# Optimization experiments

Measured on AMD Instinct MI355X. Metric: run time of the kernel, lower is better.

Reference implementation:

```python
import jax, jax.numpy as jnp
import numpy as np

B, N, D, H = 4, 2048, 256, 8
d = D // H          # 32 per-head dim
EPS = 1e-5
SCALE = 1.0 / float(np.sqrt(d))


def setup_inputs() -> dict:
    key = jax.random.key(0)
    ks = jax.random.split(key, 6)
    s = 0.02
    x = jax.random.normal(ks[0], (B, N, D), jnp.float32)
    # RoPE frequencies: theta_j = 10000^(-2j/d), angle = pos * theta
    inv_freq = 1.0 / (10000.0 ** (jnp.arange(0, d, 2, dtype=jnp.float32) / d))  # (d/2,)
    ang = jnp.arange(N, dtype=jnp.float32)[:, None] * inv_freq[None, :]          # (N, d/2)
    return {
        "x": x,
        "freqs_cos": jnp.cos(ang),
        "freqs_sin": jnp.sin(ang),
        "w_qkv": jax.random.normal(ks[1], (D, 3 * D), jnp.float32) * s,
        "b_qkv": jnp.zeros((3 * D,), jnp.float32),
        "w_proj": jax.random.normal(ks[2], (D, D), jnp.float32) * s,
        "b_proj": jnp.zeros((D,), jnp.float32),
        "ln1_g": jnp.ones((D,), jnp.float32),
        "ln1_b": jnp.zeros((D,), jnp.float32),
        "ln2_g": jnp.ones((D,), jnp.float32),
        "ln2_b": jnp.zeros((D,), jnp.float32),
        "w1": jax.random.normal(ks[3], (D, 2 * D), jnp.float32) * s,
        "b1": jnp.zeros((2 * D,), jnp.float32),
        "w2": jax.random.normal(ks[4], (2 * D, D), jnp.float32) * s,
        "b2": jnp.zeros((D,), jnp.float32),
    }


def _layer_norm(x, g, b):
    mu = jnp.mean(x, axis=-1, keepdims=True)
    var = jnp.mean(jnp.square(x - mu), axis=-1, keepdims=True)
    return (x - mu) * jax.lax.rsqrt(var + EPS) * g + b


def _rope(t, cos, sin):
    # t: (B,H,N,d); interleaved (even,odd) pairs viewed as complex, multiplied by e^{i*ang}
    tr = t.reshape(B, H, N, d // 2, 2)
    te, to = tr[..., 0], tr[..., 1]
    c = cos[None, None, :, :]
    s = sin[None, None, :, :]
    oe = te * c - to * s
    oo = te * s + to * c
    return jnp.stack([oe, oo], axis=-1).reshape(B, H, N, d)


def reference(x, freqs_cos, freqs_sin, w_qkv, b_qkv, w_proj, b_proj,
              ln1_g, ln1_b, ln2_g, ln2_b, w1, b1, w2, b2):
    # Pre-LN MHSA with RoPE (dropout = identity at eval)
    h = _layer_norm(x, ln1_g, ln1_b)
    qkv = (h @ w_qkv + b_qkv).reshape(B, N, 3, H, d).transpose(0, 2, 3, 1, 4)  # (B,3,H,N,d)
    q, k, v = qkv[:, 0], qkv[:, 1], qkv[:, 2]
    q = _rope(q, freqs_cos, freqs_sin)
    k = _rope(k, freqs_cos, freqs_sin)
    attn = jax.nn.softmax(jnp.einsum('bhnd,bhmd->bhnm', q, k) * SCALE, axis=-1)
    out = jnp.einsum('bhnm,bhmd->bhnd', attn, v).transpose(0, 2, 1, 3).reshape(B, N, D)
    x = x + (out @ w_proj + b_proj)
    h = _layer_norm(x, ln2_g, ln2_b)
    ffn = jax.nn.relu(h @ w1 + b1) @ w2 + b2
    return x + ffn
```

## Files before the change

kernel.cpp:

```cpp
#include <hip/hip_runtime.h>
#include <hip/hip_bf16.h>
#include <math.h>

#define Bsz 4
#define Nseq 2048
#define Dm 256
#define Hh 8
#define Hd 32
#define EPS_ 1e-5f
#define SCALE_ 0.17677669529663687f

typedef __attribute__((ext_vector_type(8))) short short8;
typedef __attribute__((ext_vector_type(4))) short short4v;
typedef __attribute__((ext_vector_type(4))) float f32x4;

__device__ __forceinline__ void gload16(const void* g, void* l) {
    __builtin_amdgcn_global_load_lds(
        (const __attribute__((address_space(1))) void*)g,
        (__attribute__((address_space(3))) void*)l, 16, 0, 0);
}

__device__ __forceinline__ short8 read8x2(const __hip_bfloat16* p) {
    short4v lo = *(const short4v*)p;
    short4v hi = *(const short4v*)(p + 4);
    return __builtin_shufflevector(lo, hi, 0, 1, 2, 3, 4, 5, 6, 7);
}

__global__ __launch_bounds__(256) void ln_kernel(const float* __restrict__ x,
                                                 const float* __restrict__ g,
                                                 const float* __restrict__ b,
                                                 __hip_bfloat16* __restrict__ out) {
    int row  = blockIdx.x * 4 + (threadIdx.x >> 6);
    int lane = threadIdx.x & 63;
    const float* xr = x + (size_t)row * Dm;
    float4 v = *(const float4*)(xr + lane * 4);
    float s  = v.x + v.y + v.z + v.w;
    float ss = v.x * v.x + v.y * v.y + v.z * v.z + v.w * v.w;
    #pragma unroll
    for (int off = 32; off; off >>= 1) {
        s  += __shfl_xor(s, off);
        ss += __shfl_xor(ss, off);
    }
    float mu  = s * (1.0f / Dm);
    float var = ss * (1.0f / Dm) - mu * mu;
    float rs  = rsqrtf(var + EPS_);
    float4 gv = *(const float4*)(g + lane * 4);
    float4 bv = *(const float4*)(b + lane * 4);
    float o0 = (v.x - mu) * rs * gv.x + bv.x;
    float o1 = (v.y - mu) * rs * gv.y + bv.y;
    float o2 = (v.z - mu) * rs * gv.z + bv.z;
    float o3 = (v.w - mu) * rs * gv.w + bv.w;
    __hip_bfloat16 h0 = __float2bfloat16(o0), h1 = __float2bfloat16(o1);
    __hip_bfloat16 h2 = __float2bfloat16(o2), h3 = __float2bfloat16(o3);
    short4v o4 = { *(short*)&h0, *(short*)&h1, *(short*)&h2, *(short*)&h3 };
    *(short4v*)(out + (size_t)row * Dm + lane * 4) = o4;
}

__global__ __launch_bounds__(256) void wconv_kernel(
    const float* __restrict__ s0, const float* __restrict__ s1,
    const float* __restrict__ s2, const float* __restrict__ s3,
    __hip_bfloat16* __restrict__ d0, __hip_bfloat16* __restrict__ d1,
    __hip_bfloat16* __restrict__ d2, __hip_bfloat16* __restrict__ d3) {
    __shared__ float t[32][33];
    int bid = blockIdx.x;
    const float* src; __hip_bfloat16* dst; int K, N, tb;
    if (bid < 192)      { src = s0; dst = d0; K = 256; N = 768; tb = bid; }
    else if (bid < 256) { src = s1; dst = d1; K = 256; N = 256; tb = bid - 192; }
    else if (bid < 384) { src = s2; dst = d2; K = 256; N = 512; tb = bid - 256; }
    else                { src = s3; dst = d3; K = 512; N = 256; tb = bid - 384; }
    int tn = N >> 5;
    int k0 = (tb / tn) * 32, n0 = (tb % tn) * 32;
    int c = threadIdx.x & 31, r0 = threadIdx.x >> 5;
    #pragma unroll
    for (int i = 0; i < 4; i++) {
        int r = r0 + i * 8;
        t[r][c] = src[(size_t)(k0 + r) * N + n0 + c];
    }
    __syncthreads();
    #pragma unroll
    for (int i = 0; i < 4; i++) {
        int n = r0 + i * 8;
        dst[(size_t)(n0 + n) * K + k0 + c] = __float2bfloat16(t[c][n]);
    }
}

template <int EPI>
__global__ __launch_bounds__(256) void mfma_gemm(const __hip_bfloat16* __restrict__ A,
                                                 const __hip_bfloat16* __restrict__ Wt,
                                                 const float* __restrict__ bias,
                                                 const float* __restrict__ res,
                                                 float* __restrict__ Cf,
                                                 __hip_bfloat16* __restrict__ Cb,
                                                 int M, int Nn, int K) {
    __shared__ __align__(16) __hip_bfloat16 As[128 * 32];
    __shared__ __align__(16) __hip_bfloat16 Bs[64 * 32];
    const int tid = threadIdx.x, w = tid >> 6, lane = tid & 63;
    const int lm = lane & 15, lq = lane >> 4;
    const int bm = blockIdx.y * 128, bn = blockIdx.x * 64;
    f32x4 acc[2][4];
    #pragma unroll
    for (int i = 0; i < 2; i++)
        #pragma unroll
        for (int j = 0; j < 4; j++) acc[i][j] = (f32x4){0.f, 0.f, 0.f, 0.f};

    const int sw = (lq ^ (lm & 3)) * 8;
    for (int k0 = 0; k0 < K; k0 += 32) {
        #pragma unroll
        for (int p = 0; p < 2; p++) {
            int c = p * 256 + w * 64 + lane;
            int r = c >> 2, gk = ((c & 3) ^ (r & 3)) * 8;
            gload16(A + (size_t)(bm + r) * K + k0 + gk, As + (p * 256 + w * 64) * 8);
        }
        {
            int c = w * 64 + lane;
            int r = c >> 2, gk = ((c & 3) ^ (r & 3)) * 8;
            gload16(Wt + (size_t)(bn + r) * K + k0 + gk, Bs + (w * 64) * 8);
        }
        __syncthreads();
        short8 a0 = *(const short8*)&As[(w * 32 + lm) * 32 + sw];
        short8 a1 = *(const short8*)&As[(w * 32 + 16 + lm) * 32 + sw];
        #pragma unroll
        for (int nf = 0; nf < 4; nf++) {
            short8 bfr = *(const short8*)&Bs[(nf * 16 + lm) * 32 + sw];
            acc[0][nf] = __builtin_amdgcn_mfma_f32_16x16x32_bf16(a0, bfr, acc[0][nf], 0, 0, 0);
            acc[1][nf] = __builtin_amdgcn_mfma_f32_16x16x32_bf16(a1, bfr, acc[1][nf], 0, 0, 0);
        }
        __syncthreads();
    }
    #pragma unroll
    for (int nf = 0; nf < 4; nf++) {
        int cg = bn + nf * 16 + lm;
        float bi = bias[cg];
        #pragma unroll
        for (int mf = 0; mf < 2; mf++) {
            #pragma unroll
            for (int r = 0; r < 4; r++) {
                int rg = bm + w * 32 + mf * 16 + lq * 4 + r;
                float v = acc[mf][nf][r] + bi;
                if (EPI == 1) {
                    v = fmaxf(v, 0.f);
                    Cb[(size_t)rg * Nn + cg] = __float2bfloat16(v);
                } else {
                    v += res[(size_t)rg * Nn + cg];
                    Cf[(size_t)rg * Nn + cg] = v;
                }
            }
        }
    }
}

__global__ __launch_bounds__(256) void qkv_mfma(const __hip_bfloat16* __restrict__ A,
                                                const __hip_bfloat16* __restrict__ Wt,
                                                const float* __restrict__ bias,
                                                const float* __restrict__ fcos,
                                                const float* __restrict__ fsin,
                                                __hip_bfloat16* __restrict__ qout,
                                                __hip_bfloat16* __restrict__ kout,
                                                __hip_bfloat16* __restrict__ vout) {
    const int K = 256, Nn = 768;
    __shared__ __align__(16) __hip_bfloat16 As[128 * 32];
    __shared__ __align__(16) __hip_bfloat16 Bs[64 * 32];
    __shared__ __align__(16) float cosS[2048];
    __shared__ __align__(16) float sinS[2048];
    const int tid = threadIdx.x, w = tid >> 6, lane = tid & 63;
    const int lm = lane & 15, lq = lane >> 4;
    const int bm = blockIdx.y * 128, bn = blockIdx.x * 64;
    f32x4 acc[2][4];
    #pragma unroll
    for (int i = 0; i < 2; i++)
        #pragma unroll
        for (int j = 0; j < 4; j++) acc[i][j] = (f32x4){0.f, 0.f, 0.f, 0.f};

    const int sw = (lq ^ (lm & 3)) * 8;
    for (int k0 = 0; k0 < K; k0 += 32) {
        #pragma unroll
        for (int p = 0; p < 2; p++) {
            int c = p * 256 + w * 64 + lane;
            int r = c >> 2, gk = ((c & 3) ^ (r & 3)) * 8;
            gload16(A + (size_t)(bm + r) * K + k0 + gk, As + (p * 256 + w * 64) * 8);
        }
        {
            int c = w * 64 + lane;
            int r = c >> 2, gk = ((c & 3) ^ (r & 3)) * 8;
            gload16(Wt + (size_t)(bn + r) * K + k0 + gk, Bs + (w * 64) * 8);
        }
        __syncthreads();
        short8 a0 = *(const short8*)&As[(w * 32 + lm) * 32 + sw];
        short8 a1 = *(const short8*)&As[(w * 32 + 16 + lm) * 32 + sw];
        #pragma unroll
        for (int nf = 0; nf < 4; nf++) {
            short8 bfr = *(const short8*)&Bs[(nf * 16 + lm) * 32 + sw];
            acc[0][nf] = __builtin_amdgcn_mfma_f32_16x16x32_bf16(a0, bfr, acc[0][nf], 0, 0, 0);
            acc[1][nf] = __builtin_amdgcn_mfma_f32_16x16x32_bf16(a1, bfr, acc[1][nf], 0, 0, 0);
        }
        __syncthreads();
    }
    int n0 = bm & (Nseq - 1);
    *(float4*)&cosS[tid * 8]     = *(const float4*)&fcos[n0 * 16 + tid * 8];
    *(float4*)&cosS[tid * 8 + 4] = *(const float4*)&fcos[n0 * 16 + tid * 8 + 4];
    *(float4*)&sinS[tid * 8]     = *(const float4*)&fsin[n0 * 16 + tid * 8];
    *(float4*)&sinS[tid * 8 + 4] = *(const float4*)&fsin[n0 * 16 + tid * 8 + 4];
    __syncthreads();

    const int seg = bn >> 8;
    #pragma unroll
    for (int nf = 0; nf < 4; nf++) {
        int cg = bn + nf * 16 + lm;
        int hh = (cg & 255) >> 5;
        int dd = (nf & 1) * 16 + lm;
        int i0 = dd >> 1;
        float bi = bias[cg];
        #pragma unroll
        for (int mf = 0; mf < 2; mf++) {
            #pragma unroll
            for (int r = 0; r < 4; r++) {
                int rg = bm + w * 32 + mf * 16 + lq * 4 + r;
                int nl = rg - bm;
                float v = acc[mf][nf][r] + bi;
                float vp = __shfl_xor(v, 1);
                float outv;
                if (seg < 2) {
                    float cs = cosS[nl * 16 + i0], sn = sinS[nl * 16 + i0];
                    outv = (dd & 1) ? (vp * sn + v * cs) : (v * cs - vp * sn);
                    if (seg == 0) outv *= SCALE_;
                } else {
                    outv = v;
                }
                int bb = rg >> 11, n = rg & (Nseq - 1);
                __hip_bfloat16* dst = (seg == 0) ? qout : ((seg == 1) ? kout : vout);
                dst[(((size_t)(bb * Hh + hh)) * Nseq + n) * Hd + dd] = __float2bfloat16(outv);
            }
        }
    }
}

__global__ __launch_bounds__(256) void attn_mfma(const __hip_bfloat16* __restrict__ q,
                                                 const __hip_bfloat16* __restrict__ k,
                                                 const __hip_bfloat16* __restrict__ v,
                                                 __hip_bfloat16* __restrict__ att) {
    __shared__ __align__(16) __hip_bfloat16 Qs[64 * 32];
    __shared__ __align__(16) __hip_bfloat16 Ks[2][64 * 32];
    __shared__ __align__(16) __hip_bfloat16 Vt[2][32 * 68];
    __shared__ __align__(16) __hip_bfloat16 Ps[4][16 * 68];
    const int tid = threadIdx.x, w = tid >> 6, lane = tid & 63;
    const int lm = lane & 15, lq = lane >> 4;
    const int bh = blockIdx.y, qbase = blockIdx.x * 64;
    const __hip_bfloat16* qp = q + ((size_t)bh * Nseq + qbase) * Hd;
    const __hip_bfloat16* kp = k + (size_t)bh * Nseq * Hd;
    const __hip_bfloat16* vp = v + (size_t)bh * Nseq * Hd;
    const int srow = tid >> 2, sc = tid & 3;
    const int ssw = (sc ^ (srow & 3)) * 8;

    *(float4*)&Qs[srow * 32 + sc * 8] = *(const float4*)(qp + srow * 32 + ssw);
    {
        float4 k4 = *(const float4*)(kp + srow * 32 + ssw);
        float4 v4 = *(const float4*)(vp + (size_t)srow * Hd + sc * 8);
        *(float4*)&Ks[0][srow * 32 + sc * 8] = k4;
        const __hip_bfloat16* vv = (const __hip_bfloat16*)&v4;
        #pragma unroll
        for (int j = 0; j < 8; j++) Vt[0][(sc * 8 + j) * 68 + srow] = vv[j];
    }
    __syncthreads();

    const int sw = (lq ^ (lm & 3)) * 8;
    short8 qf = *(const short8*)&Qs[(w * 16 + lm) * 32 + sw];
    f32x4 O0 = {0.f, 0.f, 0.f, 0.f};
    f32x4 O1 = {0.f, 0.f, 0.f, 0.f};
    float sm[4] = {0.f, 0.f, 0.f, 0.f};

    for (int kt = 0; kt < Nseq / 64; kt++) {
        int cur = kt & 1;
        if (kt + 1 < Nseq / 64) {
            const __hip_bfloat16* kpn = kp + (size_t)(kt + 1) * 64 * Hd;
            float4 k4 = *(const float4*)(kpn + srow * 32 + ssw);
            float4 v4 = *(const float4*)(vp + (size_t)((kt + 1) * 64 + srow) * Hd + sc * 8);
            *(float4*)&Ks[cur ^ 1][srow * 32 + sc * 8] = k4;
            const __hip_bfloat16* vv = (const __hip_bfloat16*)&v4;
            #pragma unroll
            for (int j = 0; j < 8; j++) Vt[cur ^ 1][(sc * 8 + j) * 68 + srow] = vv[j];
        }
        f32x4 S[4];
        #pragma unroll
        for (int kb = 0; kb < 4; kb++) {
            short8 kf = *(const short8*)&Ks[cur][(kb * 16 + lm) * 32 + sw];
            f32x4 zz = {0.f, 0.f, 0.f, 0.f};
            S[kb] = __builtin_amdgcn_mfma_f32_16x16x32_bf16(qf, kf, zz, 0, 0, 0);
        }
        #pragma unroll
        for (int kb = 0; kb < 4; kb++) {
            #pragma unroll
            for (int r = 0; r < 4; r++) {
                float p = __expf(S[kb][r]);
                sm[r] += p;
                Ps[w][(lq * 4 + r) * 68 + kb * 16 + lm] = __float2bfloat16(p);
            }
        }
        #pragma unroll
        for (int sub = 0; sub < 2; sub++) {
            short8 pf  = read8x2(&Ps[w][lm * 68 + sub * 32 + lq * 8]);
            short8 vf0 = read8x2(&Vt[cur][lm * 68 + sub * 32 + lq * 8]);
            short8 vf1 = read8x2(&Vt[cur][(16 + lm) * 68 + sub * 32 + lq * 8]);
            O0 = __builtin_amdgcn_mfma_f32_16x16x32_bf16(pf, vf0, O0, 0, 0, 0);
            O1 = __builtin_amdgcn_mfma_f32_16x16x32_bf16(pf, vf1, O1, 0, 0, 0);
        }
        __syncthreads();
    }
    #pragma unroll
    for (int off = 1; off <= 8; off <<= 1) {
        #pragma unroll
        for (int r = 0; r < 4; r++) sm[r] += __shfl_xor(sm[r], off);
    }
    const int bb = bh >> 3, hh = bh & 7;
    #pragma unroll
    for (int r = 0; r < 4; r++) {
        float inv = 1.0f / sm[r];
        int n = qbase + w * 16 + lq * 4 + r;
        __hip_bfloat16* op = att + ((size_t)(bb * Nseq + n)) * Dm + hh * Hd;
        op[lm]      = __float2bfloat16(O0[r] * inv);
        op[16 + lm] = __float2bfloat16(O1[r] * inv);
    }
}

extern "C" void kernel_launch(void* const* d_in, const int* in_sizes, int n_in,
                              void* d_out, int out_size, void* d_ws, size_t ws_size,
                              hipStream_t stream) {
    const float* x      = (const float*)d_in[0];
    const float* fcos   = (const float*)d_in[1];
    const float* fsin   = (const float*)d_in[2];
    const float* w_qkv  = (const float*)d_in[3];
    const float* b_qkv  = (const float*)d_in[4];
    const float* w_proj = (const float*)d_in[5];
    const float* b_proj = (const float*)d_in[6];
    const float* ln1_g  = (const float*)d_in[7];
    const float* ln1_b  = (const float*)d_in[8];
    const float* ln2_g  = (const float*)d_in[9];
    const float* ln2_b  = (const float*)d_in[10];
    const float* w1     = (const float*)d_in[11];
    const float* b1     = (const float*)d_in[12];
    const float* w2     = (const float*)d_in[13];
    const float* b2     = (const float*)d_in[14];
    float* out = (float*)d_out;
    char* base = (char*)d_ws;
    const size_t MB = (size_t)1 << 20;

    __hip_bfloat16* h   = (__hip_bfloat16*)(base);
    float*          x2f = (float*)(base);
    __hip_bfloat16* qb  = (__hip_bfloat16*)(base + 8 * MB);
    __hip_bfloat16* kbf = (__hip_bfloat16*)(base + 12 * MB);
    __hip_bfloat16* vbf = (__hip_bfloat16*)(base + 16 * MB);
    __hip_bfloat16* att = (__hip_bfloat16*)(base + 20 * MB);
    __hip_bfloat16* h2  = (__hip_bfloat16*)(base + 8 * MB);
    __hip_bfloat16* ffn = (__hip_bfloat16*)(base + 24 * MB);
    __hip_bfloat16* wqT = (__hip_bfloat16*)(base + 32 * MB);
    __hip_bfloat16* wpT = (__hip_bfloat16*)(base + 32 * MB + 393216);
    __hip_bfloat16* w1T = (__hip_bfloat16*)(base + 32 * MB + 524288);
    __hip_bfloat16* w2T = (__hip_bfloat16*)(base + 32 * MB + 786432);

    const int rows = Bsz * Nseq;

    wconv_kernel<<<512, 256, 0, stream>>>(w_qkv, w_proj, w1, w2, wqT, wpT, w1T, w2T);
    ln_kernel<<<rows / 4, 256, 0, stream>>>(x, ln1_g, ln1_b, h);
    qkv_mfma<<<dim3(12, 64), 256, 0, stream>>>(h, wqT, b_qkv, fcos, fsin, qb, kbf, vbf);
    attn_mfma<<<dim3(Nseq / 64, Bsz * Hh), 256, 0, stream>>>(qb, kbf, vbf, att);
    mfma_gemm<2><<<dim3(4, 64), 256, 0, stream>>>(att, wpT, b_proj, x, x2f, nullptr,
                                                  rows, 256, 256);
    ln_kernel<<<rows / 4, 256, 0, stream>>>(x2f, ln2_g, ln2_b, h2);
    mfma_gemm<1><<<dim3(8, 64), 256, 0, stream>>>(h2, w1T, b1, nullptr, nullptr, ffn,
                                                  rows, 512, 256);
    mfma_gemm<2><<<dim3(4, 64), 256, 0, stream>>>(ffn, w2T, b2, x2f, out, nullptr,
                                                  rows, 256, 512);
}
```

Before: 192.6 us.

## Fuse LayerNorm into QKV/FFN1 GEMMs, pre-transpose V, shrink proj/FFN2 tiles

LayerNorm is folded into the QKV and FFN1 GEMM prologues: per-row statistics are computed into shared memory and the A tile is normalized and converted to bf16 on the fly, which removes two separate LN kernels and their bf16 intermediates. The QKV epilogue writes V already transposed, so attention can load V fragments straight into registers and load Q/K with async global-to-LDS copies instead of scattering into LDS. The proj and FFN2 GEMMs move to 64-row tiles to double the block count. In exchange each QKV/FFN1 block re-reads fp32 x from global memory for every output column tile, and the RoPE tables are now read from global memory instead of shared memory.

After: 230.3 us. 1.2x slower.

```diff
diff --git a/kernel.cpp b/kernel.cpp
--- a/kernel.cpp
+++ b/kernel.cpp
@@ -26,34 +26,9 @@
     return __builtin_shufflevector(lo, hi, 0, 1, 2, 3, 4, 5, 6, 7);
 }
 
-__global__ __launch_bounds__(256) void ln_kernel(const float* __restrict__ x,
-                                                 const float* __restrict__ g,
-                                                 const float* __restrict__ b,
-                                                 __hip_bfloat16* __restrict__ out) {
-    int row  = blockIdx.x * 4 + (threadIdx.x >> 6);
-    int lane = threadIdx.x & 63;
-    const float* xr = x + (size_t)row * Dm;
-    float4 v = *(const float4*)(xr + lane * 4);
-    float s  = v.x + v.y + v.z + v.w;
-    float ss = v.x * v.x + v.y * v.y + v.z * v.z + v.w * v.w;
-    #pragma unroll
-    for (int off = 32; off; off >>= 1) {
-        s  += __shfl_xor(s, off);
-        ss += __shfl_xor(ss, off);
-    }
-    float mu  = s * (1.0f / Dm);
-    float var = ss * (1.0f / Dm) - mu * mu;
-    float rs  = rsqrtf(var + EPS_);
-    float4 gv = *(const float4*)(g + lane * 4);
-    float4 bv = *(const float4*)(b + lane * 4);
-    float o0 = (v.x - mu) * rs * gv.x + bv.x;
-    float o1 = (v.y - mu) * rs * gv.y + bv.y;
-    float o2 = (v.z - mu) * rs * gv.z + bv.z;
-    float o3 = (v.w - mu) * rs * gv.w + bv.w;
-    __hip_bfloat16 h0 = __float2bfloat16(o0), h1 = __float2bfloat16(o1);
-    __hip_bfloat16 h2 = __float2bfloat16(o2), h3 = __float2bfloat16(o3);
-    short4v o4 = { *(short*)&h0, *(short*)&h1, *(short*)&h2, *(short*)&h3 };
-    *(short4v*)(out + (size_t)row * Dm + lane * 4) = o4;
+__device__ __forceinline__ short bf16s(float f) {
+    __hip_bfloat16 h = __float2bfloat16(f);
+    return *(short*)&h;
 }
 
 __global__ __launch_bounds__(256) void wconv_kernel(
@@ -84,7 +59,7 @@
     }
 }
 
-template <int EPI>
+template <int TM, int EPI>
 __global__ __launch_bounds__(256) void mfma_gemm(const __hip_bfloat16* __restrict__ A,
                                                  const __hip_bfloat16* __restrict__ Wt,
                                                  const float* __restrict__ bias,
@@ -92,38 +67,41 @@
                                                  float* __restrict__ Cf,
                                                  __hip_bfloat16* __restrict__ Cb,
                                                  int M, int Nn, int K) {
-    __shared__ __align__(16) __hip_bfloat16 As[128 * 32];
+    constexpr int MF = TM / 64;
+    __shared__ __align__(16) __hip_bfloat16 As[TM * 32];
     __shared__ __align__(16) __hip_bfloat16 Bs[64 * 32];
     const int tid = threadIdx.x, w = tid >> 6, lane = tid & 63;
     const int lm = lane & 15, lq = lane >> 4;
-    const int bm = blockIdx.y * 128, bn = blockIdx.x * 64;
-    f32x4 acc[2][4];
-    #pragma unroll
-    for (int i = 0; i < 2; i++)
+    const int bm = blockIdx.y * TM, bn = blockIdx.x * 64;
+    f32x4 acc[MF][4];
+    #pragma unroll
+    for (int i = 0; i < MF; i++)
         #pragma unroll
         for (int j = 0; j < 4; j++) acc[i][j] = (f32x4){0.f, 0.f, 0.f, 0.f};
 
     const int sw = (lq ^ (lm & 3)) * 8;
     for (int k0 = 0; k0 < K; k0 += 32) {
         #pragma unroll
-        for (int p = 0; p < 2; p++) {
-            int c = p * 256 + w * 64 + lane;
+        for (int p = 0; p < MF; p++) {
+            int c = p * 256 + tid;
             int r = c >> 2, gk = ((c & 3) ^ (r & 3)) * 8;
             gload16(A + (size_t)(bm + r) * K + k0 + gk, As + (p * 256 + w * 64) * 8);
         }
         {
-            int c = w * 64 + lane;
-            int r = c >> 2, gk = ((c & 3) ^ (r & 3)) * 8;
-            gload16(Wt + (size_t)(bn + r) * K + k0 + gk, Bs + (w * 64) * 8);
-        }
-        __syncthreads();
-        short8 a0 = *(const short8*)&As[(w * 32 + lm) * 32 + sw];
-        short8 a1 = *(const short8*)&As[(w * 32 + 16 + lm) * 32 + sw];
+            int r = tid >> 2, gk = ((tid & 3) ^ (r & 3)) * 8;
+            gload16(Wt + (size_t)(bn + r) * K + k0 + gk, Bs + w * 512);
+        }
+        __syncthreads();
+        short8 a[MF];
+        #pragma unroll
+        for (int mf = 0; mf < MF; mf++)
+            a[mf] = *(const short8*)&As[(w * (TM / 4) + mf * 16 + lm) * 32 + sw];
         #pragma unroll
         for (int nf = 0; nf < 4; nf++) {
             short8 bfr = *(const short8*)&Bs[(nf * 16 + lm) * 32 + sw];
-            acc[0][nf] = __builtin_amdgcn_mfma_f32_16x16x32_bf16(a0, bfr, acc[0][nf], 0, 0, 0);
-            acc[1][nf] = __builtin_amdgcn_mfma_f32_16x16x32_bf16(a1, bfr, acc[1][nf], 0, 0, 0);
+            #pragma unroll
+            for (int mf = 0; mf < MF; mf++)
+                acc[mf][nf] = __builtin_amdgcn_mfma_f32_16x16x32_bf16(a[mf], bfr, acc[mf][nf], 0, 0, 0);
         }
         __syncthreads();
     }
@@ -132,10 +110,10 @@
         int cg = bn + nf * 16 + lm;
         float bi = bias[cg];
         #pragma unroll
-        for (int mf = 0; mf < 2; mf++) {
+        for (int mf = 0; mf < MF; mf++) {
             #pragma unroll
             for (int r = 0; r < 4; r++) {
-                int rg = bm + w * 32 + mf * 16 + lq * 4 + r;
+                int rg = bm + w * (TM / 4) + mf * 16 + lq * 4 + r;
                 float v = acc[mf][nf][r] + bi;
                 if (EPI == 1) {
                     v = fmaxf(v, 0.f);
@@ -149,22 +127,48 @@
     }
 }
 
-__global__ __launch_bounds__(256) void qkv_mfma(const __hip_bfloat16* __restrict__ A,
-                                                const __hip_bfloat16* __restrict__ Wt,
-                                                const float* __restrict__ bias,
-                                                const float* __restrict__ fcos,
-                                                const float* __restrict__ fsin,
-                                                __hip_bfloat16* __restrict__ qout,
-                                                __hip_bfloat16* __restrict__ kout,
-                                                __hip_bfloat16* __restrict__ vout) {
-    const int K = 256, Nn = 768;
+__global__ __launch_bounds__(256) void qkv_fused(const float* __restrict__ x,
+                                                 const __hip_bfloat16* __restrict__ Wt,
+                                                 const float* __restrict__ bias,
+                                                 const float* __restrict__ g,
+                                                 const float* __restrict__ bvec,
+                                                 const float* __restrict__ fcos,
+                                                 const float* __restrict__ fsin,
+                                                 __hip_bfloat16* __restrict__ qout,
+                                                 __hip_bfloat16* __restrict__ kout,
+                                                 __hip_bfloat16* __restrict__ vt) {
+    const int K = 256;
     __shared__ __align__(16) __hip_bfloat16 As[128 * 32];
     __shared__ __align__(16) __hip_bfloat16 Bs[64 * 32];
-    __shared__ __align__(16) float cosS[2048];
-    __shared__ __align__(16) float sinS[2048];
+    __shared__ float muS[128], rsS[128];
     const int tid = threadIdx.x, w = tid >> 6, lane = tid & 63;
     const int lm = lane & 15, lq = lane >> 4;
     const int bm = blockIdx.y * 128, bn = blockIdx.x * 64;
+
+    #pragma unroll
+    for (int i = 0; i < 8; i++) {
+        int r = w * 32 + i * 4 + (lane >> 4);
+        const float* xr = x + (size_t)(bm + r) * 256 + (lane & 15) * 16;
+        float s = 0.f, ss = 0.f;
+        #pragma unroll
+        for (int j = 0; j < 4; j++) {
+            float4 v = *(const float4*)(xr + j * 4);
+            s  += v.x + v.y + v.z + v.w;
+            ss += v.x * v.x + v.y * v.y + v.z * v.z + v.w * v.w;
+        }
+        #pragma unroll
+        for (int off = 1; off <= 8; off <<= 1) {
+            s  += __shfl_xor(s, off);
+            ss += __shfl_xor(ss, off);
+        }
+        if ((lane & 15) == 0) {
+            float mu = s * (1.0f / 256.0f);
+            muS[r] = mu;
+            rsS[r] = rsqrtf(ss * (1.0f / 256.0f) - mu * mu + EPS_);
+        }
+    }
+    __syncthreads();
+
     f32x4 acc[2][4];
     #pragma unroll
     for (int i = 0; i < 2; i++)
@@ -173,16 +177,40 @@
 
     const int sw = (lq ^ (lm & 3)) * 8;
     for (int k0 = 0; k0 < K; k0 += 32) {
+        short8 hbuf[2];
+        int rr[2];
         #pragma unroll
         for (int p = 0; p < 2; p++) {
-            int c = p * 256 + w * 64 + lane;
+            int c = p * 256 + tid;
             int r = c >> 2, gk = ((c & 3) ^ (r & 3)) * 8;
-            gload16(A + (size_t)(bm + r) * K + k0 + gk, As + (p * 256 + w * 64) * 8);
+            rr[p] = r;
+            const float* src = x + (size_t)(bm + r) * 256 + k0 + gk;
+            float4 f0 = *(const float4*)src;
+            float4 f1 = *(const float4*)(src + 4);
+            float4 g0 = *(const float4*)(g + k0 + gk);
+            float4 g1 = *(const float4*)(g + k0 + gk + 4);
+            float4 b0 = *(const float4*)(bvec + k0 + gk);
+            float4 b1 = *(const float4*)(bvec + k0 + gk + 4);
+            float mu = muS[r], rs = rsS[r];
+            short8 h;
+            h[0] = bf16s((f0.x - mu) * rs * g0.x + b0.x);
+            h[1] = bf16s((f0.y - mu) * rs * g0.y + b0.y);
+            h[2] = bf16s((f0.z - mu) * rs * g0.z + b0.z);
+            h[3] = bf16s((f0.w - mu) * rs * g0.w + b0.w);
+            h[4] = bf16s((f1.x - mu) * rs * g1.x + b1.x);
+            h[5] = bf16s((f1.y - mu) * rs * g1.y + b1.y);
+            h[6] = bf16s((f1.z - mu) * rs * g1.z + b1.z);
+            h[7] = bf16s((f1.w - mu) * rs * g1.w + b1.w);
+            hbuf[p] = h;
         }
         {
-            int c = w * 64 + lane;
-            int r = c >> 2, gk = ((c & 3) ^ (r & 3)) * 8;
-            gload16(Wt + (size_t)(bn + r) * K + k0 + gk, Bs + (w * 64) * 8);
+            int r = tid >> 2, gk = ((tid & 3) ^ (r & 3)) * 8;
+            gload16(Wt + (size_t)(bn + r) * K + k0 + gk, Bs + w * 512);
+        }
+        #pragma unroll
+        for (int p = 0; p < 2; p++) {
+            int c = p * 256 + tid;
+            *(short8*)&As[(rr[p] * 4 + (c & 3)) * 8] = hbuf[p];
         }
         __syncthreads();
         short8 a0 = *(const short8*)&As[(w * 32 + lm) * 32 + sw];
@@ -195,13 +223,6 @@
         }
         __syncthreads();
     }
-    int n0 = bm & (Nseq - 1);
-    *(float4*)&cosS[tid * 8]     = *(const float4*)&fcos[n0 * 16 + tid * 8];
-    *(float4*)&cosS[tid * 8 + 4] = *(const float4*)&fcos[n0 * 16 + tid * 8 + 4];
-    *(float4*)&sinS[tid * 8]     = *(const float4*)&fsin[n0 * 16 + tid * 8];
-    *(float4*)&sinS[tid * 8 + 4] = *(const float4*)&fsin[n0 * 16 + tid * 8 + 4];
-    __syncthreads();
-
     const int seg = bn >> 8;
     #pragma unroll
     for (int nf = 0; nf < 4; nf++) {
@@ -215,20 +236,127 @@
             #pragma unroll
             for (int r = 0; r < 4; r++) {
                 int rg = bm + w * 32 + mf * 16 + lq * 4 + r;
-                int nl = rg - bm;
+                int bb = rg >> 11, n = rg & (Nseq - 1);
                 float v = acc[mf][nf][r] + bi;
-                float vp = __shfl_xor(v, 1);
-                float outv;
-                if (seg < 2) {
-                    float cs = cosS[nl * 16 + i0], sn = sinS[nl * 16 + i0];
-                    outv = (dd & 1) ? (vp * sn + v * cs) : (v * cs - vp * sn);
+                if (seg == 2) {
+                    vt[(((size_t)(bb * Hh + hh)) * Hd + dd) * Nseq + n] = __float2bfloat16(v);
+                } else {
+                    float vp = __shfl_xor(v, 1);
+                    float cs = fcos[n * 16 + i0], sn = fsin[n * 16 + i0];
+                    float outv = (dd & 1) ? (vp * sn + v * cs) : (v * cs - vp * sn);
                     if (seg == 0) outv *= SCALE_;
-                } else {
-                    outv = v;
+                    __hip_bfloat16* dst = (seg == 0) ? qout : kout;
+                    dst[(((size_t)(bb * Hh + hh)) * Nseq + n) * Hd + dd] = __float2bfloat16(outv);
                 }
-                int bb = rg >> 11, n = rg & (Nseq - 1);
-                __hip_bfloat16* dst = (seg == 0) ? qout : ((seg == 1) ? kout : vout);
-                dst[(((size_t)(bb * Hh + hh)) * Nseq + n) * Hd + dd] = __float2bfloat16(outv);
+            }
+        }
+    }
+}
+
+__global__ __launch_bounds__(256) void ffn1_fused(const float* __restrict__ x,
+                                                  const __hip_bfloat16* __restrict__ Wt,
+                                                  const float* __restrict__ bias,
+                                                  const float* __restrict__ g,
+                                                  const float* __restrict__ bvec,
+                                                  __hip_bfloat16* __restrict__ Cb,
+                                                  int Nn) {
+    const int K = 256;
+    __shared__ __align__(16) __hip_bfloat16 As[128 * 32];
+    __shared__ __align__(16) __hip_bfloat16 Bs[64 * 32];
+    __shared__ float muS[128], rsS[128];
+    const int tid = threadIdx.x, w = tid >> 6, lane = tid & 63;
+    const int lm = lane & 15, lq = lane >> 4;
+    const int bm = blockIdx.y * 128, bn = blockIdx.x * 64;
+
+    #pragma unroll
+    for (int i = 0; i < 8; i++) {
+        int r = w * 32 + i * 4 + (lane >> 4);
+        const float* xr = x + (size_t)(bm + r) * 256 + (lane & 15) * 16;
+        float s = 0.f, ss = 0.f;
+        #pragma unroll
+        for (int j = 0; j < 4; j++) {
+            float4 v = *(const float4*)(xr + j * 4);
+            s  += v.x + v.y + v.z + v.w;
+            ss += v.x * v.x + v.y * v.y + v.z * v.z + v.w * v.w;
+        }
+        #pragma unroll
+        for (int off = 1; off <= 8; off <<= 1) {
+            s  += __shfl_xor(s, off);
+            ss += __shfl_xor(ss, off);
+        }
+        if ((lane & 15) == 0) {
+            float mu = s * (1.0f / 256.0f);
+            muS[r] = mu;
+            rsS[r] = rsqrtf(ss * (1.0f / 256.0f) - mu * mu + EPS_);
+        }
+    }
+    __syncthreads();
+
+    f32x4 acc[2][4];
+    #pragma unroll
+    for (int i = 0; i < 2; i++)
+        #pragma unroll
+        for (int j = 0; j < 4; j++) acc[i][j] = (f32x4){0.f, 0.f, 0.f, 0.f};
+
+    const int sw = (lq ^ (lm & 3)) * 8;
+    for (int k0 = 0; k0 < K; k0 += 32) {
+        short8 hbuf[2];
+        int rr[2];
+        #pragma unroll
+        for (int p = 0; p < 2; p++) {
+            int c = p * 256 + tid;
+            int r = c >> 2, gk = ((c & 3) ^ (r & 3)) * 8;
+            rr[p] = r;
+            const float* src = x + (size_t)(bm + r) * 256 + k0 + gk;
+            float4 f0 = *(const float4*)src;
+            float4 f1 = *(const float4*)(src + 4);
+            float4 g0 = *(const float4*)(g + k0 + gk);
+            float4 g1 = *(const float4*)(g + k0 + gk + 4);
+            float4 b0 = *(const float4*)(bvec + k0 + gk);
+            float4 b1 = *(const float4*)(bvec + k0 + gk + 4);
+            float mu = muS[r], rs = rsS[r];
+            short8 h;
+            h[0] = bf16s((f0.x - mu) * rs * g0.x + b0.x);
+            h[1] = bf16s((f0.y - mu) * rs * g0.y + b0.y);
+            h[2] = bf16s((f0.z - mu) * rs * g0.z + b0.z);
+            h[3] = bf16s((f0.w - mu) * rs * g0.w + b0.w);
+            h[4] = bf16s((f1.x - mu) * rs * g1.x + b1.x);
+            h[5] = bf16s((f1.y - mu) * rs * g1.y + b1.y);
+            h[6] = bf16s((f1.z - mu) * rs * g1.z + b1.z);
+            h[7] = bf16s((f1.w - mu) * rs * g1.w + b1.w);
+            hbuf[p] = h;
+        }
+        {
+            int r = tid >> 2, gk = ((tid & 3) ^ (r & 3)) * 8;
+            gload16(Wt + (size_t)(bn + r) * K + k0 + gk, Bs + w * 512);
+        }
+        #pragma unroll
+        for (int p = 0; p < 2; p++) {
+            int c = p * 256 + tid;
+            *(short8*)&As[(rr[p] * 4 + (c & 3)) * 8] = hbuf[p];
+        }
+        __syncthreads();
+        short8 a0 = *(const short8*)&As[(w * 32 + lm) * 32 + sw];
+        short8 a1 = *(const short8*)&As[(w * 32 + 16 + lm) * 32 + sw];
+        #pragma unroll
+        for (int nf = 0; nf < 4; nf++) {
+            short8 bfr = *(const short8*)&Bs[(nf * 16 + lm) * 32 + sw];
+            acc[0][nf] = __builtin_amdgcn_mfma_f32_16x16x32_bf16(a0, bfr, acc[0][nf], 0, 0, 0);
+            acc[1][nf] = __builtin_amdgcn_mfma_f32_16x16x32_bf16(a1, bfr, acc[1][nf], 0, 0, 0);
+        }
+        __syncthreads();
+    }
+    #pragma unroll
+    for (int nf = 0; nf < 4; nf++) {
+        int cg = bn + nf * 16 + lm;
+        float bi = bias[cg];
+        #pragma unroll
+        for (int mf = 0; mf < 2; mf++) {
+            #pragma unroll
+            for (int r = 0; r < 4; r++) {
+                int rg = bm + w * 32 + mf * 16 + lq * 4 + r;
+                float v = fmaxf(acc[mf][nf][r] + bi, 0.f);
+                Cb[(size_t)rg * Nn + cg] = __float2bfloat16(v);
             }
         }
     }
@@ -236,30 +364,26 @@
 
 __global__ __launch_bounds__(256) void attn_mfma(const __hip_bfloat16* __restrict__ q,
                                                  const __hip_bfloat16* __restrict__ k,
-                                                 const __hip_bfloat16* __restrict__ v,
+                                                 const __hip_bfloat16* __restrict__ vt,
                                                  __hip_bfloat16* __restrict__ att) {
     __shared__ __align__(16) __hip_bfloat16 Qs[64 * 32];
     __shared__ __align__(16) __hip_bfloat16 Ks[2][64 * 32];
-    __shared__ __align__(16) __hip_bfloat16 Vt[2][32 * 68];
     __shared__ __align__(16) __hip_bfloat16 Ps[4][16 * 68];
     const int tid = threadIdx.x, w = tid >> 6, lane = tid & 63;
     const int lm = lane & 15, lq = lane >> 4;
     const int bh = blockIdx.y, qbase = blockIdx.x * 64;
-    const __hip_bfloat16* qp = q + ((size_t)bh * Nseq + qbase) * Hd;
-    const __hip_bfloat16* kp = k + (size_t)bh * Nseq * Hd;
-    const __hip_bfloat16* vp = v + (size_t)bh * Nseq * Hd;
-    const int srow = tid >> 2, sc = tid & 3;
-    const int ssw = (sc ^ (srow & 3)) * 8;
-
-    *(float4*)&Qs[srow * 32 + sc * 8] = *(const float4*)(qp + srow * 32 + ssw);
-    {
-        float4 k4 = *(const float4*)(kp + srow * 32 + ssw);
-        float4 v4 = *(const float4*)(vp + (size_t)srow * Hd + sc * 8);
-        *(float4*)&Ks[0][srow * 32 + sc * 8] = k4;
-        const __hip_bfloat16* vv = (const __hip_bfloat16*)&v4;
-        #pragma unroll
-        for (int j = 0; j < 8; j++) Vt[0][(sc * 8 + j) * 68 + srow] = vv[j];
-    }
+    const __hip_bfloat16* qp  = q + ((size_t)bh * Nseq + qbase) * Hd;
+    const __hip_bfloat16* kp  = k + (size_t)bh * Nseq * Hd;
+    const __hip_bfloat16* vr0 = vt + ((size_t)bh * Hd + lm) * Nseq + lq * 8;
+    const __hip_bfloat16* vr1 = vr0 + 16 * Nseq;
+
+    const int sr = tid >> 2, sgk = ((tid & 3) ^ (sr & 3)) * 8;
+    gload16(qp + sr * 32 + sgk, Qs + w * 512);
+    gload16(kp + sr * 32 + sgk, Ks[0] + w * 512);
+    short8 v00 = *(const short8*)(vr0);
+    short8 v01 = *(const short8*)(vr0 + 32);
+    short8 v10 = *(const short8*)(vr1);
+    short8 v11 = *(const short8*)(vr1 + 32);
     __syncthreads();
 
     const int sw = (lq ^ (lm & 3)) * 8;
@@ -270,14 +394,14 @@
 
     for (int kt = 0; kt < Nseq / 64; kt++) {
         int cur = kt & 1;
+        short8 n00, n01, n10, n11;
         if (kt + 1 < Nseq / 64) {
-            const __hip_bfloat16* kpn = kp + (size_t)(kt + 1) * 64 * Hd;
-            float4 k4 = *(const float4*)(kpn + srow * 32 + ssw);
-            float4 v4 = *(const float4*)(vp + (size_t)((kt + 1) * 64 + srow) * Hd + sc * 8);
-            *(float4*)&Ks[cur ^ 1][srow * 32 + sc * 8] = k4;
-            const __hip_bfloat16* vv = (const __hip_bfloat16*)&v4;
-            #pragma unroll
-            for (int j = 0; j < 8; j++) Vt[cur ^ 1][(sc * 8 + j) * 68 + srow] = vv[j];
+            gload16(kp + (size_t)(kt + 1) * 64 * 32 + sr * 32 + sgk, Ks[cur ^ 1] + w * 512);
+            int kb = (kt + 1) * 64;
+            n00 = *(const short8*)(vr0 + kb);
+            n01 = *(const short8*)(vr0 + kb + 32);
+            n10 = *(const short8*)(vr1 + kb);
+            n11 = *(const short8*)(vr1 + kb + 32);
         }
         f32x4 S[4];
         #pragma unroll
@@ -295,14 +419,13 @@
                 Ps[w][(lq * 4 + r) * 68 + kb * 16 + lm] = __float2bfloat16(p);
             }
         }
-        #pragma unroll
-        for (int sub = 0; sub < 2; sub++) {
-            short8 pf  = read8x2(&Ps[w][lm * 68 + sub * 32 + lq * 8]);
-            short8 vf0 = read8x2(&Vt[cur][lm * 68 + sub * 32 + lq * 8]);
-            short8 vf1 = read8x2(&Vt[cur][(16 + lm) * 68 + sub * 32 + lq * 8]);
-            O0 = __builtin_amdgcn_mfma_f32_16x16x32_bf16(pf, vf0, O0, 0, 0, 0);
-            O1 = __builtin_amdgcn_mfma_f32_16x16x32_bf16(pf, vf1, O1, 0, 0, 0);
-        }
+        short8 pf0 = read8x2(&Ps[w][lm * 68 + lq * 8]);
+        short8 pf1 = read8x2(&Ps[w][lm * 68 + 32 + lq * 8]);
+        O0 = __builtin_amdgcn_mfma_f32_16x16x32_bf16(pf0, v00, O0, 0, 0, 0);
+        O1 = __builtin_amdgcn_mfma_f32_16x16x32_bf16(pf0, v10, O1, 0, 0, 0);
+        O0 = __builtin_amdgcn_mfma_f32_16x16x32_bf16(pf1, v01, O0, 0, 0, 0);
+        O1 = __builtin_amdgcn_mfma_f32_16x16x32_bf16(pf1, v11, O1, 0, 0, 0);
+        v00 = n00; v01 = n01; v10 = n10; v11 = n11;
         __syncthreads();
     }
     #pragma unroll
@@ -343,13 +466,11 @@
     char* base = (char*)d_ws;
     const size_t MB = (size_t)1 << 20;
 
-    __hip_bfloat16* h   = (__hip_bfloat16*)(base);
-    float*          x2f = (float*)(base);
-    __hip_bfloat16* qb  = (__hip_bfloat16*)(base + 8 * MB);
-    __hip_bfloat16* kbf = (__hip_bfloat16*)(base + 12 * MB);
-    __hip_bfloat16* vbf = (__hip_bfloat16*)(base + 16 * MB);
-    __hip_bfloat16* att = (__hip_bfloat16*)(base + 20 * MB);
-    __hip_bfloat16* h2  = (__hip_bfloat16*)(base + 8 * MB);
+    __hip_bfloat16* qb  = (__hip_bfloat16*)(base);
+    __hip_bfloat16* kbf = (__hip_bfloat16*)(base + 4 * MB);
+    __hip_bfloat16* vtb = (__hip_bfloat16*)(base + 8 * MB);
+    __hip_bfloat16* att = (__hip_bfloat16*)(base + 12 * MB);
+    float*          x2f = (float*)(base + 16 * MB);
     __hip_bfloat16* ffn = (__hip_bfloat16*)(base + 24 * MB);
     __hip_bfloat16* wqT = (__hip_bfloat16*)(base + 32 * MB);
     __hip_bfloat16* wpT = (__hip_bfloat16*)(base + 32 * MB + 393216);
@@ -359,14 +480,12 @@
     const int rows = Bsz * Nseq;
 
     wconv_kernel<<<512, 256, 0, stream>>>(w_qkv, w_proj, w1, w2, wqT, wpT, w1T, w2T);
-    ln_kernel<<<rows / 4, 256, 0, stream>>>(x, ln1_g, ln1_b, h);
-    qkv_mfma<<<dim3(12, 64), 256, 0, stream>>>(h, wqT, b_qkv, fcos, fsin, qb, kbf, vbf);
-    attn_mfma<<<dim3(Nseq / 64, Bsz * Hh), 256, 0, stream>>>(qb, kbf, vbf, att);
-    mfma_gemm<2><<<dim3(4, 64), 256, 0, stream>>>(att, wpT, b_proj, x, x2f, nullptr,
-                                                  rows, 256, 256);
-    ln_kernel<<<rows / 4, 256, 0, stream>>>(x2f, ln2_g, ln2_b, h2);
-    mfma_gemm<1><<<dim3(8, 64), 256, 0, stream>>>(h2, w1T, b1, nullptr, nullptr, ffn,
-                                                  rows, 512, 256);
-    mfma_gemm<2><<<dim3(4, 64), 256, 0, stream>>>(ffn, w2T, b2, x2f, out, nullptr,
-                                                  rows, 256, 512);
-}
+    qkv_fused<<<dim3(12, 64), 256, 0, stream>>>(x, wqT, b_qkv, ln1_g, ln1_b, fcos, fsin,
+                                                qb, kbf, vtb);
+    attn_mfma<<<dim3(Nseq / 64, Bsz * Hh), 256, 0, stream>>>(qb, kbf, vtb, att);
+    mfma_gemm<64, 2><<<dim3(4, 128), 256, 0, stream>>>(att, wpT, b_proj, x, x2f, nullptr,
+                                                       rows, 256, 256);
+    ffn1_fused<<<dim3(8, 64), 256, 0, stream>>>(x2f, w1T, b1, ln2_g, ln2_b, ffn, 512);
+    mfma_gemm<64, 2><<<dim3(4, 128), 256, 0, stream>>>(ffn, w2T, b2, x2f, out,
+                                                       nullptr, rows, 256, 512);
+}
```
